# Kernel tuning notes

Hardware: AMD Instinct MI355X
Metric: run time of the kernel (lower is better)

The kernel has to match this reference:

```python
import jax, jax.numpy as jnp
import numpy as np

B, S, H = 4, 4096, 4096
E, G, TOPK_GROUP, TOP_K = 160, 8, 3, 6
SCALE = 16.0      # routed_scaling_factor (norm_topk_prob=False)
ALPHA = 0.001     # aux_loss_alpha
M = 3             # config.M for communication aux loss


def setup_inputs() -> dict:
    key = jax.random.key(0)
    k1, k2 = jax.random.split(key)
    hidden_states = jax.random.normal(k1, (B, S, H), dtype=jnp.float32)
    # kaiming_uniform_(a=sqrt(5)) on (E, H): bound = 1/sqrt(fan_in)
    bound = 1.0 / np.sqrt(H)
    weight = jax.random.uniform(k2, (E, H), minval=-bound, maxval=bound, dtype=jnp.float32)
    return {"hidden_states": hidden_states, "weight": weight}


def _gate(hidden_states, weight):
    b, s, h = hidden_states.shape
    x = hidden_states.reshape(-1, h).astype(jnp.float32)          # [T, H]
    logits = x @ weight.astype(jnp.float32).T                      # [T, E]
    scores = jax.nn.softmax(logits, axis=-1)
    T = b * s
    # group-limited greedy top-k
    group_scores = scores.reshape(T, G, E // G).max(axis=-1)       # [T, G]
    _, group_idx = jax.lax.top_k(group_scores, TOPK_GROUP)         # [T, topk_group]
    group_mask = jnp.zeros((T, G), scores.dtype).at[
        jnp.arange(T)[:, None], group_idx].set(1.0)                # [T, G]
    score_mask = jnp.repeat(group_mask, E // G, axis=1)            # [T, E]
    tmp_scores = jnp.where(score_mask > 0, scores, 0.0)
    topk_weight, topk_idx = jax.lax.top_k(tmp_scores, TOP_K)       # [T, k]
    topk_weight = topk_weight * SCALE
    # --- aux losses (training, seq_aux=True, alpha>0) ---
    idx_flat = topk_idx.reshape(b, s * TOP_K)                      # [b, s*k]
    counts = jax.vmap(
        lambda idx: jnp.zeros((E,), jnp.float32).at[idx].add(1.0)
    )(idx_flat)                                                    # [b, E]
    ce = counts / (s * TOP_K / E)
    mean_scores = scores.reshape(b, s, E).mean(axis=1)             # [b, E]
    aux_expert = (ce * mean_scores).sum(axis=1).mean() * ALPHA
    ce_g = ce.reshape(b, G, -1).mean(axis=-1)                      # [b, G]
    ms_g = mean_scores.reshape(b, G, -1).mean(axis=-1)             # [b, G]
    aux_device = (ce_g * ms_g).sum(axis=1).mean() * ALPHA
    ce2 = counts.reshape(b, G, -1).sum(axis=-1) / (M * s / G)      # [b, G]
    aux_comm = (ce2 * ms_g).sum(axis=1).mean() * ALPHA
    aux_loss = aux_expert + aux_device + aux_comm
    return topk_idx, topk_weight, aux_loss


def reference(hidden_states, weight):
    return _gate(hidden_states, weight)
```

## Files before the change

kernel.cpp:

```cpp
#include <hip/hip_runtime.h>

typedef _Float16 half8 __attribute__((ext_vector_type(8)));
typedef float f32x4 __attribute__((ext_vector_type(4)));

#define H    4096
#define NE   160
#define BM   32
#define TPB  256
#define NIT  64


__global__ __launch_bounds__(256) void prep_kernel(
    const float* __restrict__ w, _Float16* __restrict__ Wf)
{
    int F    = blockIdx.x * 256 + threadIdx.x;
    int lane = F & 63;
    int t10  = (F >> 6) % 10;
    int ks   = F / 640;
    int e    = t10 * 16 + (lane & 15);
    int k0   = ks * 32 + (lane >> 4) * 8;
    const float* p = w + (size_t)e * H + k0;
    float4 v0 = *(const float4*)p;
    float4 v1 = *(const float4*)(p + 4);
    float vv[8] = {v0.x, v0.y, v0.z, v0.w, v1.x, v1.y, v1.z, v1.w};
    half8 h0, h1;
#pragma unroll
    for (int j = 0; j < 8; ++j) {
        float s = vv[j] * 64.f;
        _Float16 a = (_Float16)s;
        h0[j] = a;
        h1[j] = (_Float16)((s - (float)a) * 2048.f);
    }
    half8* out = (half8*)Wf;
    out[(ks * 20 + t10) * 64 + lane]      = h0;
    out[(ks * 20 + 10 + t10) * 64 + lane] = h1;
}

#define GLOAD_LDS(SRC, DST)                                                    \
    __builtin_amdgcn_global_load_lds(                                          \
        (const __attribute__((address_space(1))) unsigned int*)(SRC),          \
        (__attribute__((address_space(3))) unsigned int*)(DST), 16, 0, 0)

#define CONVERT(U0, U1)                                                        \
    do {                                                                       \
        float v0=U0.x, v1=U0.y, v2=U0.z, v3=U0.w;                              \
        float v4=U1.x, v5=U1.y, v6=U1.z, v7=U1.w;                              \
        _Float16 h;                                                            \
        h=(_Float16)v0; a0[0]=h; a1[0]=(_Float16)((v0-(float)h)*2048.f);       \
        h=(_Float16)v1; a0[1]=h; a1[1]=(_Float16)((v1-(float)h)*2048.f);       \
        h=(_Float16)v2; a0[2]=h; a1[2]=(_Float16)((v2-(float)h)*2048.f);       \
        h=(_Float16)v3; a0[3]=h; a1[3]=(_Float16)((v3-(float)h)*2048.f);       \
        h=(_Float16)v4; a0[4]=h; a1[4]=(_Float16)((v4-(float)h)*2048.f);       \
        h=(_Float16)v5; a0[5]=h; a1[5]=(_Float16)((v5-(float)h)*2048.f);       \
        h=(_Float16)v6; a0[6]=h; a1[6]=(_Float16)((v6-(float)h)*2048.f);       \
        h=(_Float16)v7; a0[7]=h; a1[7]=(_Float16)((v7-(float)h)*2048.f);       \
    } while (0)

__global__ __launch_bounds__(TPB) void gate_kernel(
    const float* __restrict__ x, const _Float16* __restrict__ Wf,
    float* __restrict__ outIdx, float* __restrict__ outW,
    float* __restrict__ gcnt, float* __restrict__ gssum)
{
    __shared__ __align__(16) _Float16 s_stage[2560 * 8];
    __shared__ float s_mx[BM], s_inv[BM];
    __shared__ int   s_cnt[NE];
    float* s_log = (float*)s_stage;

    const int tid  = threadIdx.x;
    const int lane = tid & 63;
    const int wv   = tid >> 6;
    const int nh   = wv & 1;
    const int kh   = wv >> 1;
    const int row0 = blockIdx.x * BM;
    const int rql  = lane & 15;
    const int kq   = (lane >> 4) * 8;

    if (tid < NE) s_cnt[tid] = 0;

    f32x4 accH[2][5], accL[2][5];
#pragma unroll
    for (int g = 0; g < 2; ++g)
#pragma unroll
        for (int t = 0; t < 5; ++t) { accH[g][t] = (f32x4){0,0,0,0}; accL[g][t] = (f32x4){0,0,0,0}; }

    const float* xp0 = x + (size_t)(row0 + rql) * H + kh * 32 + kq;
    const float* xp1 = xp0 + (size_t)16 * H;
    const int sbase = kh * 1280 + nh * 5 * 64 + lane;

    for (int it = 0; it < NIT; ++it) {
        __syncthreads();

        {
            const _Float16* srcH = Wf + ((size_t)it * 2560 + tid) * 8;
            _Float16*       dstH = s_stage + (size_t)tid * 8;
#pragma unroll
            for (int i = 0; i < 10; ++i)
                GLOAD_LDS(srcH + i * 2048, dstH + i * 2048);
        }
        float4 u00 = *(const float4*)(xp0 + (size_t)it * 64);
        float4 u01 = *(const float4*)(xp0 + (size_t)it * 64 + 4);
        float4 u10 = *(const float4*)(xp1 + (size_t)it * 64);
        float4 u11 = *(const float4*)(xp1 + (size_t)it * 64 + 4);

        __syncthreads();

        const half8* B = (const half8*)s_stage + sbase;
        half8 b0[5], b1[5];
#pragma unroll
        for (int t = 0; t < 5; ++t) { b0[t] = B[t * 64]; b1[t] = B[640 + t * 64]; }

        half8 a0, a1;
        CONVERT(u00, u01);
#pragma unroll
        for (int t = 0; t < 5; ++t) {
            accH[0][t] = __builtin_amdgcn_mfma_f32_16x16x32_f16(a0, b0[t], accH[0][t], 0, 0, 0);
            accL[0][t] = __builtin_amdgcn_mfma_f32_16x16x32_f16(a1, b0[t], accL[0][t], 0, 0, 0);
            accL[0][t] = __builtin_amdgcn_mfma_f32_16x16x32_f16(a0, b1[t], accL[0][t], 0, 0, 0);
        }
        CONVERT(u10, u11);
#pragma unroll
        for (int t = 0; t < 5; ++t) {
            accH[1][t] = __builtin_amdgcn_mfma_f32_16x16x32_f16(a0, b0[t], accH[1][t], 0, 0, 0);
            accL[1][t] = __builtin_amdgcn_mfma_f32_16x16x32_f16(a1, b0[t], accL[1][t], 0, 0, 0);
            accL[1][t] = __builtin_amdgcn_mfma_f32_16x16x32_f16(a0, b1[t], accL[1][t], 0, 0, 0);
        }
    }

    __syncthreads();

    const int crow  = (lane >> 4) * 4;
    const int ccol0 = nh * 80 + (lane & 15);
    if (kh == 0) {
#pragma unroll
        for (int g = 0; g < 2; ++g)
#pragma unroll
            for (int t = 0; t < 5; ++t)
#pragma unroll
                for (int r = 0; r < 4; ++r)
                    s_log[(g * 16 + crow + r) * 161 + ccol0 + t * 16] =
                        (accH[g][t][r] + accL[g][t][r] * (1.0f / 2048.f)) * (1.0f / 64.f);
    }
    __syncthreads();
    if (kh == 1) {
#pragma unroll
        for (int g = 0; g < 2; ++g)
#pragma unroll
            for (int t = 0; t < 5; ++t)
#pragma unroll
                for (int r = 0; r < 4; ++r)
                    s_log[(g * 16 + crow + r) * 161 + ccol0 + t * 16] +=
                        (accH[g][t][r] + accL[g][t][r] * (1.0f / 2048.f)) * (1.0f / 64.f);
    }
    __syncthreads();

    if (tid < BM) {
        const float* L = &s_log[tid * 161];
        float gmax[8];
        float mx = -3.4e38f;
#pragma unroll
        for (int g = 0; g < 8; ++g) {
            float m = L[g * 20];
            for (int j = 1; j < 20; ++j) m = fmaxf(m, L[g * 20 + j]);
            gmax[g] = m;
            mx = fmaxf(mx, m);
        }
        float sum = 0.f;
        for (int e = 0; e < NE; ++e) sum += __expf(L[e] - mx);
        float inv = 1.0f / sum;
        s_mx[tid]  = mx;
        s_inv[tid] = inv;

        unsigned sel = 0;
        float pv = 3.4e38f; int pi = -1;
        for (int it = 0; it < 3; ++it) {
            float bv = -3.4e38f; int bi = 0;
            for (int g = 0; g < 8; ++g) {
                float v = gmax[g];
                bool below = (v < pv) || (v == pv && g > pi);
                if (below && v > bv) { bv = v; bi = g; }
            }
            sel |= 1u << bi;
            pv = bv; pi = bi;
        }

        const int tok = row0 + tid;
        float pv2 = 3.4e38f; int pi2 = -1;
        for (int it = 0; it < 6; ++it) {
            float bv = -3.4e38f; int bi = 0;
            for (int g = 0; g < 8; ++g) {
                if (!((sel >> g) & 1u)) continue;
                for (int j = 0; j < 20; ++j) {
                    int e = g * 20 + j;
                    float v = L[e];
                    bool below = (v < pv2) || (v == pv2 && e > pi2);
                    if (below && v > bv) { bv = v; bi = e; }
                }
            }
            pv2 = bv; pi2 = bi;
            outIdx[(size_t)tok * 6 + it] = (float)bi;
            outW[(size_t)tok * 6 + it]   = __expf(bv - mx) * inv * 16.0f;
            atomicAdd(&s_cnt[bi], 1);
        }
    }
    __syncthreads();

    if (tid < NE) {
        float ss = 0.f;
        for (int t2 = 0; t2 < BM; ++t2)
            ss += __expf(s_log[t2 * 161 + tid] - s_mx[t2]) * s_inv[t2];
        const int b = row0 >> 12;
        atomicAdd(&gssum[b * NE + tid], ss);
        atomicAdd(&gcnt[b * NE + tid], (float)s_cnt[tid]);
    }
}

__global__ __launch_bounds__(64) void aux_kernel(
    const float* __restrict__ gcnt, const float* __restrict__ gssum,
    float* __restrict__ out)
{
    const int lane = threadIdx.x;
    float part = 0.f;
    if (lane < 32) {
        const int b = lane >> 3, g = lane & 7;
        const float* cn = gcnt  + b * NE + g * 20;
        const float* sm = gssum + b * NE + g * 20;
        float s1 = 0.f, sc = 0.f, sms = 0.f;
        for (int j = 0; j < 20; ++j) {
            float ce = cn[j] * (1.0f / 153.6f);
            float ms = sm[j] * (1.0f / 4096.0f);
            s1  += ce * ms;
            sc  += cn[j];
            sms += ms;
        }
        float ceg = sc * (1.0f / 153.6f) * (1.0f / 20.0f);
        float msg = sms * (1.0f / 20.0f);
        float ce2 = sc * (1.0f / 1536.0f);
        part = s1 + ceg * msg + ce2 * msg;
    }
#pragma unroll
    for (int off = 32; off > 0; off >>= 1) part += __shfl_down(part, off);
    if (lane == 0) out[0] = part * (0.001f * 0.25f);
}

extern "C" void kernel_launch(void* const* d_in, const int* in_sizes, int n_in,
                              void* d_out, int out_size, void* d_ws, size_t ws_size,
                              hipStream_t stream)
{
    (void)in_sizes; (void)n_in; (void)out_size; (void)ws_size;
    const float* x = (const float*)d_in[0];
    const float* w = (const float*)d_in[1];
    float* out = (float*)d_out;

    _Float16* Wf  = (_Float16*)d_ws;
    float* gcnt  = (float*)(Wf + (size_t)NE * H * 2);
    float* gssum = gcnt + 4 * NE;

    hipMemsetAsync(gcnt, 0, 2 * 4 * NE * sizeof(float), stream);

    prep_kernel<<<(NE * H / 8) / 256, 256, 0, stream>>>(w, Wf);
    gate_kernel<<<16384 / BM, TPB, 0, stream>>>(
        x, Wf, out, out + 98304, gcnt, gssum);
    aux_kernel<<<1, 64, 0, stream>>>(gcnt, gssum, out + 196608);
}
```

Measured before the change: 238.1 us.

## Split gate GEMM row tiles across 8 waves per block

```diff
diff --git a/kernel.cpp b/kernel.cpp
--- a/kernel.cpp
+++ b/kernel.cpp
@@ -6,7 +6,7 @@
 #define H    4096
 #define NE   160
 #define BM   32
-#define TPB  256
+#define TPB  512
 #define NIT  64
 
 
@@ -69,23 +69,20 @@
     const int tid  = threadIdx.x;
     const int lane = tid & 63;
     const int wv   = tid >> 6;
+    const int kh   = wv >> 2;
+    const int mh   = (wv >> 1) & 1;
     const int nh   = wv & 1;
-    const int kh   = wv >> 1;
     const int row0 = blockIdx.x * BM;
-    const int rql  = lane & 15;
-    const int kq   = (lane >> 4) * 8;
 
     if (tid < NE) s_cnt[tid] = 0;
 
-    f32x4 accH[2][5], accL[2][5];
-#pragma unroll
-    for (int g = 0; g < 2; ++g)
-#pragma unroll
-        for (int t = 0; t < 5; ++t) { accH[g][t] = (f32x4){0,0,0,0}; accL[g][t] = (f32x4){0,0,0,0}; }
-
-    const float* xp0 = x + (size_t)(row0 + rql) * H + kh * 32 + kq;
-    const float* xp1 = xp0 + (size_t)16 * H;
-    const int sbase = kh * 1280 + nh * 5 * 64 + lane;
+    f32x4 accH[5], accL[5];
+#pragma unroll
+    for (int t = 0; t < 5; ++t) { accH[t] = (f32x4){0,0,0,0}; accL[t] = (f32x4){0,0,0,0}; }
+
+    const float* xp = x + (size_t)(row0 + mh * 16 + (lane & 15)) * H
+                        + kh * 32 + (lane >> 4) * 8;
+    const int sbase = kh * 1280 + nh * 320 + lane;
 
     for (int it = 0; it < NIT; ++it) {
         __syncthreads();
@@ -94,13 +91,11 @@
             const _Float16* srcH = Wf + ((size_t)it * 2560 + tid) * 8;
             _Float16*       dstH = s_stage + (size_t)tid * 8;
 #pragma unroll
-            for (int i = 0; i < 10; ++i)
-                GLOAD_LDS(srcH + i * 2048, dstH + i * 2048);
-        }
-        float4 u00 = *(const float4*)(xp0 + (size_t)it * 64);
-        float4 u01 = *(const float4*)(xp0 + (size_t)it * 64 + 4);
-        float4 u10 = *(const float4*)(xp1 + (size_t)it * 64);
-        float4 u11 = *(const float4*)(xp1 + (size_t)it * 64 + 4);
+            for (int i = 0; i < 5; ++i)
+                GLOAD_LDS(srcH + i * 4096, dstH + i * 4096);
+        }
+        float4 u0 = *(const float4*)(xp + (size_t)it * 64);
+        float4 u1 = *(const float4*)(xp + (size_t)it * 64 + 4);
 
         __syncthreads();
 
@@ -110,46 +105,35 @@
         for (int t = 0; t < 5; ++t) { b0[t] = B[t * 64]; b1[t] = B[640 + t * 64]; }
 
         half8 a0, a1;
-        CONVERT(u00, u01);
+        CONVERT(u0, u1);
 #pragma unroll
         for (int t = 0; t < 5; ++t) {
-            accH[0][t] = __builtin_amdgcn_mfma_f32_16x16x32_f16(a0, b0[t], accH[0][t], 0, 0, 0);
-            accL[0][t] = __builtin_amdgcn_mfma_f32_16x16x32_f16(a1, b0[t], accL[0][t], 0, 0, 0);
-            accL[0][t] = __builtin_amdgcn_mfma_f32_16x16x32_f16(a0, b1[t], accL[0][t], 0, 0, 0);
-        }
-        CONVERT(u10, u11);
-#pragma unroll
-        for (int t = 0; t < 5; ++t) {
-            accH[1][t] = __builtin_amdgcn_mfma_f32_16x16x32_f16(a0, b0[t], accH[1][t], 0, 0, 0);
-            accL[1][t] = __builtin_amdgcn_mfma_f32_16x16x32_f16(a1, b0[t], accL[1][t], 0, 0, 0);
-            accL[1][t] = __builtin_amdgcn_mfma_f32_16x16x32_f16(a0, b1[t], accL[1][t], 0, 0, 0);
-        }
-    }
-
-    __syncthreads();
-
-    const int crow  = (lane >> 4) * 4;
+            accH[t] = __builtin_amdgcn_mfma_f32_16x16x32_f16(a0, b0[t], accH[t], 0, 0, 0);
+            accL[t] = __builtin_amdgcn_mfma_f32_16x16x32_f16(a1, b0[t], accL[t], 0, 0, 0);
+            accL[t] = __builtin_amdgcn_mfma_f32_16x16x32_f16(a0, b1[t], accL[t], 0, 0, 0);
+        }
+    }
+
+    __syncthreads();
+
+    const int crow  = mh * 16 + (lane >> 4) * 4;
     const int ccol0 = nh * 80 + (lane & 15);
     if (kh == 0) {
 #pragma unroll
-        for (int g = 0; g < 2; ++g)
-#pragma unroll
-            for (int t = 0; t < 5; ++t)
-#pragma unroll
-                for (int r = 0; r < 4; ++r)
-                    s_log[(g * 16 + crow + r) * 161 + ccol0 + t * 16] =
-                        (accH[g][t][r] + accL[g][t][r] * (1.0f / 2048.f)) * (1.0f / 64.f);
+        for (int t = 0; t < 5; ++t)
+#pragma unroll
+            for (int r = 0; r < 4; ++r)
+                s_log[(crow + r) * 161 + ccol0 + t * 16] =
+                    (accH[t][r] + accL[t][r] * (1.0f / 2048.f)) * (1.0f / 64.f);
     }
     __syncthreads();
     if (kh == 1) {
 #pragma unroll
-        for (int g = 0; g < 2; ++g)
-#pragma unroll
-            for (int t = 0; t < 5; ++t)
-#pragma unroll
-                for (int r = 0; r < 4; ++r)
-                    s_log[(g * 16 + crow + r) * 161 + ccol0 + t * 16] +=
-                        (accH[g][t][r] + accL[g][t][r] * (1.0f / 2048.f)) * (1.0f / 64.f);
+        for (int t = 0; t < 5; ++t)
+#pragma unroll
+            for (int r = 0; r < 4; ++r)
+                s_log[(crow + r) * 161 + ccol0 + t * 16] +=
+                    (accH[t][r] + accL[t][r] * (1.0f / 2048.f)) * (1.0f / 64.f);
     }
     __syncthreads();
 
```

Result: no change. 242.4 us (+1.8%).
